# Performance work log

Hardware: AMD Instinct MI355X
Metric: run time of the kernel (lower is better)

The kernel has to match this reference:

```python
import jax, jax.numpy as jnp
import numpy as np

K = 16  # neighbors

def setup_inputs() -> dict:
    key = jax.random.key(0)
    k1, k2, k3 = jax.random.split(key, 3)
    B, C_in, C_out, N = 4, 64, 64, 8192
    x = jax.random.normal(k1, (B, C_in, N), dtype=jnp.float32)
    coords = jax.random.normal(k2, (B, 3, N), dtype=jnp.float32)
    W = jax.random.normal(k3, (C_out, C_in), dtype=jnp.float32) * 0.05
    return {"x": x, "coords": coords, "W": W}


def _knn_indices(coords, k):
    # coords: [B, 3, N]; squared pairwise distances d[b,i,j] = ||c_i - c_j||^2
    sq = jnp.sum(coords * coords, axis=1)                      # [B, N]
    inner = jnp.einsum('bdi,bdj->bij', coords, coords)         # [B, N, N]
    dist = sq[:, :, None] + sq[:, None, :] - 2.0 * inner       # [B, N, N]
    # k smallest distances -> top_k of negated distances
    _, idx = jax.lax.top_k(-dist, k)                           # [B, N, k]
    return idx


def _gather_neighbors(x, idx):
    # x: [B, C, N], idx: [B, N, k] -> [B, C, N, k]
    return jax.vmap(lambda xb, ib: xb[:, ib])(x, idx)


def reference(x, coords, W):
    idx = _knn_indices(coords, K)                              # [B, N, k]
    knn_x = _gather_neighbors(x, idx)                          # [B, C_in, N, k]
    # PointwiseConv2D (1x1 conv, no bias) == channel matmul
    mlp = jnp.einsum('oc,bcnk->bonk', W, knn_x)                # [B, C_out, N, k]
    y = jnp.max(mlp, axis=-1)                                  # [B, C_out, N]
    return (y, coords)
```

## Files before the change

kernel.cpp:

```cpp
#include <hip/hip_runtime.h>

#define BB 4
#define NN 8192
#define QB 32
#define NW 8
#define CAP 96
#define SLACK 6e-3f

typedef unsigned long long u64;
typedef unsigned int u32;
typedef _Float16 f16x8 __attribute__((ext_vector_type(8)));
typedef float f32x16 __attribute__((ext_vector_type(16)));

__device__ __forceinline__ u64 shfl_xor_u64(u64 v, int m) {
  u32 lo = (u32)v, hi = (u32)(v >> 32);
  lo = (u32)__shfl_xor((int)lo, m, 64);
  hi = (u32)__shfl_xor((int)hi, m, 64);
  return ((u64)hi << 32) | lo;
}
__device__ __forceinline__ u64 shfl_u64(u64 v, int src) {
  u32 lo = (u32)v, hi = (u32)(v >> 32);
  lo = (u32)__shfl((int)lo, src, 64);
  hi = (u32)__shfl((int)hi, src, 64);
  return ((u64)hi << 32) | lo;
}
__device__ __forceinline__ u64 min_u64(u64 a, u64 b) { return a < b ? a : b; }
__device__ __forceinline__ float rfl(float x) {
  return __int_as_float(__builtin_amdgcn_readfirstlane(__float_as_int(x)));
}

__device__ __forceinline__ u64 bitonic64(u64 v, int lane) {
#pragma unroll
  for (int k = 2; k <= 64; k <<= 1) {
#pragma unroll
    for (int jm = k >> 1; jm >= 1; jm >>= 1) {
      u64 o = shfl_xor_u64(v, jm);
      bool keepmin = ((lane & jm) == 0) == ((lane & k) == 0);
      u64 mn = min_u64(v, o);
      u64 mx = (v < o) ? o : v;
      v = keepmin ? mn : mx;
    }
  }
  return v;
}

__device__ __forceinline__ float dist_exact(float qx, float qy, float qz, float qw,
                                            float cx, float cy, float cz, float cw) {
#pragma clang fp contract(off)
  float inner = qx * cx;
  inner = inner + qy * cy;
  inner = inner + qz * cz;
  float tt = qw + cw;
  return __builtin_fmaf(-2.0f, inner, tt);
}

__global__ void fused_prep_zmat(const float* __restrict__ x, const float* __restrict__ W,
                                const float* __restrict__ coords,
                                float* __restrict__ z, float4* __restrict__ c4p,
                                _Float16* __restrict__ bfr,
                                float* __restrict__ ycoords) {
#pragma clang fp contract(off)
  __shared__ float Ws[64 * 65];
  __shared__ float xs[64 * 32];
  int t = threadIdx.x;
  if (blockIdx.x < 1024) {
    int blk = blockIdx.x;
    int b = blk >> 8;
    int j0 = (blk & 255) * 32;
    for (int r = t; r < 4096; r += 256) Ws[(r >> 6) * 65 + (r & 63)] = W[r];
    const float* xb = x + (size_t)b * 64 * NN;
    for (int r = 0; r < 8; ++r) {
      int idx = t + r * 256;
      int c = idx >> 5, j = idx & 31;
      xs[c * 32 + j] = xb[(size_t)c * NN + j0 + j];
    }
    __syncthreads();
    int o = t & 63, jb = (t >> 6) * 8;
    float acc[8];
#pragma unroll
    for (int m = 0; m < 8; ++m) acc[m] = 0.f;
    for (int c = 0; c < 64; ++c) {
      float w = Ws[o * 65 + c];
#pragma unroll
      for (int m = 0; m < 8; ++m) acc[m] = __builtin_fmaf(w, xs[c * 32 + jb + m], acc[m]);
    }
#pragma unroll
    for (int m = 0; m < 8; ++m)
      z[((size_t)b * NN + j0 + jb + m) * 64 + o] = acc[m];
  } else {
    int t2 = (blockIdx.x - 1024) * 256 + t;
    int b = t2 >> 13;
    int i = t2 & (NN - 1);
    const float* cb = coords + (size_t)b * 3 * NN;
    float cx = cb[i];
    float cy = cb[NN + i];
    float cz = cb[2 * NN + i];
    float sq = (cx * cx + cy * cy) + cz * cz;
    float4 v; v.x = -2.0f * cx; v.y = -2.0f * cy; v.z = -2.0f * cz; v.w = sq;
    c4p[t2] = v;

    _Float16 xh = (_Float16)v.x, yh = (_Float16)v.y, zh = (_Float16)v.z;
    _Float16 xl = (_Float16)(v.x - (float)xh);
    _Float16 yl = (_Float16)(v.y - (float)yh);
    _Float16 zl = (_Float16)(v.z - (float)zh);
    _Float16 sh = (_Float16)sq;
    _Float16 sl = (_Float16)(sq - (float)sh);
    f16x8 b0, b1;
    b0[0] = xh; b0[1] = xh; b0[2] = xl; b0[3] = yh;
    b0[4] = yh; b0[5] = yl; b0[6] = zh; b0[7] = zh;
    b1[0] = zl; b1[1] = sh; b1[2] = sl;
    b1[3] = (_Float16)0.f; b1[4] = (_Float16)0.f; b1[5] = (_Float16)0.f;
    b1[6] = (_Float16)0.f; b1[7] = (_Float16)0.f;
    f16x8* bp = (f16x8*)bfr;
    bp[(size_t)t2 * 2]     = b0;
    bp[(size_t)t2 * 2 + 1] = b1;

#pragma unroll
    for (int r = 0; r < 3; ++r)
      ycoords[r * (BB * NN) + t2] = coords[r * (BB * NN) + t2];
  }
}

__global__ void __launch_bounds__(512, 8) knn_gather(const float4* __restrict__ c4p,
                                                     const _Float16* __restrict__ bfr,
                                                     const float* __restrict__ z,
                                                     float* __restrict__ y) {
  __shared__ __align__(16) char pool[QB * 128 * 4];
  __shared__ float TfL[QB];
  __shared__ int scnt[QB];
  __shared__ int sidx[QB][16];
  __shared__ float ys[64][QB + 1];
  float (*wmin)[128] = (float(*)[128])pool;
  u32 (*survj)[CAP] = (u32(*)[CAP])pool;

  int t = threadIdx.x;
  int w = t >> 6, lane = t & 63;
  int lq = lane & 31, lg = lane >> 5;
  int lg4 = lg << 2;
  int qbase = blockIdx.x * QB;
  int b = qbase >> 13;
  int i0 = qbase & (NN - 1);
  const float4* cp = c4p + (size_t)b * NN;
  int wbase = w * (NN / NW);

  if (t < QB) scnt[t] = 0;

  float4 qv = cp[i0 + lq];
  float qx = -0.5f * qv.x, qy = -0.5f * qv.y, qz = -0.5f * qv.z;
  _Float16 xh = (_Float16)qx, yh = (_Float16)qy, zh = (_Float16)qz;
  _Float16 xl = (_Float16)(qx - (float)xh);
  _Float16 yl = (_Float16)(qy - (float)yh);
  _Float16 zl = (_Float16)(qz - (float)zh);
  f16x8 af;
  if (lg == 0) {
    af[0] = xh; af[1] = xl; af[2] = xh; af[3] = yh;
    af[4] = yl; af[5] = yh; af[6] = zh; af[7] = zl;
  } else {
    af[0] = zh; af[1] = (_Float16)1.0f; af[2] = (_Float16)1.0f;
    af[3] = (_Float16)0.f; af[4] = (_Float16)0.f; af[5] = (_Float16)0.f;
    af[6] = (_Float16)0.f; af[7] = (_Float16)0.f;
  }

  f32x16 zzz, mn;
#pragma unroll
  for (int r = 0; r < 16; ++r) { zzz[r] = 0.f; mn[r] = 3.402823466e+38f; }

  const f16x8* lp = (const f16x8*)bfr + (((size_t)b * NN + wbase + lq) * 2 + lg);

#pragma unroll 2
  for (int tt = 0; tt < 32; tt += 2) {
    f16x8 bc0 = lp[tt * 64];
    f16x8 bc1 = lp[(tt + 1) * 64];
    f32x16 d0 = __builtin_amdgcn_mfma_f32_32x32x16_f16(af, bc0, zzz, 0, 0, 0);
    f32x16 d1 = __builtin_amdgcn_mfma_f32_32x32x16_f16(af, bc1, zzz, 0, 0, 0);
#pragma unroll
    for (int r = 0; r < 16; ++r) mn[r] = fminf(fminf(mn[r], d0[r]), d1[r]);
  }

#pragma unroll
  for (int r = 0; r < 16; ++r) {
    float m2 = fminf(mn[r], __shfl_xor(mn[r], 16, 64));
    int q = (r & 3) + 8 * (r >> 2) + lg4;
    if (lq < 16) wmin[q][w * 16 + lq] = m2;
  }
  __syncthreads();

#pragma unroll 1
  for (int qi = 0; qi < QB / NW; ++qi) {
    int q = w * (QB / NW) + qi;
    float v = fminf(wmin[q][2 * lane], wmin[q][2 * lane + 1]);
#pragma unroll
    for (int k = 2; k <= 64; k <<= 1) {
#pragma unroll
      for (int jm = k >> 1; jm >= 1; jm >>= 1) {
        float o = __shfl_xor(v, jm, 64);
        bool keepmin = ((lane & jm) == 0) == ((lane & k) == 0);
        v = keepmin ? fminf(v, o) : fmaxf(v, o);
      }
    }
    if (lane == 15) TfL[q] = v + SLACK;
  }
  __syncthreads();

  f32x16 mc;
#pragma unroll
  for (int r = 0; r < 16; ++r) mc[r] = -TfL[(r & 3) + 8 * (r >> 2) + lg4];

#pragma unroll 2
  for (int tt = 0; tt < 32; ++tt) {
    f16x8 bc = lp[tt * 64];
    f32x16 d = __builtin_amdgcn_mfma_f32_32x32x16_f16(af, bc, mc, 0, 0, 0);
    int cand = wbase + tt * 32 + lq;
#pragma unroll
    for (int r = 0; r < 16; ++r) {
      if (d[r] <= 0.f) {
        int q = (r & 3) + 8 * (r >> 2) + lg4;
        int pos = atomicAdd(&scnt[q], 1);
        if (pos < CAP) survj[q][pos] = (u32)cand;
      }
    }
  }
  __syncthreads();

  const float* zb = z + (size_t)b * NN * 64;
#pragma unroll 1
  for (int qi = 0; qi < QB / NW; ++qi) {
    int q = w * (QB / NW) + qi;
    int n = scnt[q]; if (n > CAP) n = CAP;
    float4 qq = cp[i0 + q];
    float eqx = rfl(-0.5f * qq.x), eqy = rfl(-0.5f * qq.y);
    float eqz = rfl(-0.5f * qq.z), eqw = rfl(qq.w);
    u64 v = ~0ull;
    if (lane < n) {
      int c = (int)survj[q][lane];
      float4 cj = cp[c];
      float de = dist_exact(eqx, eqy, eqz, eqw,
                            -0.5f * cj.x, -0.5f * cj.y, -0.5f * cj.z, cj.w);
      u32 f = __float_as_uint(de);
      u32 m32 = f ^ ((u32)(((int)f) >> 31) | 0x80000000u);
      v = ((u64)m32 << 32) | (u32)c;
    }
    v = bitonic64(v, lane);
    if (n > 64) {
      u64 v2 = ~0ull;
      if (lane + 64 < n) {
        int c = (int)survj[q][lane + 64];
        float4 cj = cp[c];
        float de = dist_exact(eqx, eqy, eqz, eqw,
                              -0.5f * cj.x, -0.5f * cj.y, -0.5f * cj.z, cj.w);
        u32 f = __float_as_uint(de);
        u32 m32 = f ^ ((u32)(((int)f) >> 31) | 0x80000000u);
        v2 = ((u64)m32 << 32) | (u32)c;
      }
      v2 = bitonic64(v2, lane);
      u64 vm = (lane < 16) ? v : ((lane < 32) ? shfl_u64(v2, lane - 16) : ~0ull);
      v = bitonic64(vm, lane);
    }
    if (lane < 16) sidx[q][lane] = (int)(v & 0xFFFFFFFFull);
  }

#pragma unroll 1
  for (int qi = 0; qi < QB / NW; ++qi) {
    int q = w * (QB / NW) + qi;
    const int* id = sidx[q];
    float m = -3.402823466e+38f;
#pragma unroll
    for (int k = 0; k < 16; ++k)
      m = fmaxf(m, zb[(size_t)id[k] * 64 + lane]);
    ys[lane][q] = m;
  }
  __syncthreads();
  {
    int o = t >> 3;
    int ql0 = (t & 7) * 4;
    float4 vv;
    vv.x = ys[o][ql0]; vv.y = ys[o][ql0 + 1];
    vv.z = ys[o][ql0 + 2]; vv.w = ys[o][ql0 + 3];
    *(float4*)&y[((size_t)b * 64 + o) * NN + i0 + ql0] = vv;
  }
}

extern "C" void kernel_launch(void* const* d_in, const int* in_sizes, int n_in,
                              void* d_out, int out_size, void* d_ws, size_t ws_size,
                              hipStream_t stream) {
  const float* x      = (const float*)d_in[0];
  const float* coords = (const float*)d_in[1];
  const float* W      = (const float*)d_in[2];
  float* y = (float*)d_out;

  char* ws = (char*)d_ws;
  float4*   c4p = (float4*)ws;
  _Float16* bfr = (_Float16*)(ws + (512u << 10));
  float*    z   = (float*)(ws + (2u << 20));

  float* ycoords = y + (size_t)BB * 64 * NN;

  fused_prep_zmat<<<1024 + 128, 256, 0, stream>>>(x, W, coords, z, c4p, bfr, ycoords);
  knn_gather<<<BB * NN / QB, 512, 0, stream>>>(c4p, bfr, z, y);
}
```

Before: 137.7 us.

## Register-tile the z matmul and sample fewer candidates for the kNN threshold

The prep kernel's channel matmul moves to 64-point blocks with a 4x4 register tile per thread. It reads a transposed, padded W and x tiles from shared memory as float4 and writes z with float4 stores, which halves the prep grid. In the kNN kernel, the first pass that estimates each query's distance threshold now scans only half the candidate tiles, and the survivor-collection loop is unrolled further. The shuffle used when merging the two sorted survivor halves is now done by every lane instead of inside a divergent select. Sampling fewer candidates gives a looser threshold, so more points survive, which risks overflowing the fixed survivor capacity and costs extra exact-distance sorting work.

```diff
diff --git a/kernel.cpp b/kernel.cpp
--- a/kernel.cpp
+++ b/kernel.cpp
@@ -54,41 +54,59 @@
   return __builtin_fmaf(-2.0f, inner, tt);
 }
 
-__global__ void fused_prep_zmat(const float* __restrict__ x, const float* __restrict__ W,
-                                const float* __restrict__ coords,
-                                float* __restrict__ z, float4* __restrict__ c4p,
-                                _Float16* __restrict__ bfr,
-                                float* __restrict__ ycoords) {
+__global__ void __launch_bounds__(256, 4) fused_prep_zmat(
+    const float* __restrict__ x, const float* __restrict__ W,
+    const float* __restrict__ coords,
+    float* __restrict__ z, float4* __restrict__ c4p,
+    _Float16* __restrict__ bfr,
+    float* __restrict__ ycoords) {
 #pragma clang fp contract(off)
-  __shared__ float Ws[64 * 65];
-  __shared__ float xs[64 * 32];
+  __shared__ float Wst[64 * 68];
+  __shared__ float xs[64 * 64];
   int t = threadIdx.x;
-  if (blockIdx.x < 1024) {
+  if (blockIdx.x < 512) {
     int blk = blockIdx.x;
-    int b = blk >> 8;
-    int j0 = (blk & 255) * 32;
-    for (int r = t; r < 4096; r += 256) Ws[(r >> 6) * 65 + (r & 63)] = W[r];
+    int b = blk >> 7;
+    int j0 = (blk & 127) * 64;
+    for (int r = t; r < 4096; r += 256) Wst[(r & 63) * 68 + (r >> 6)] = W[r];
     const float* xb = x + (size_t)b * 64 * NN;
-    for (int r = 0; r < 8; ++r) {
+#pragma unroll
+    for (int r = 0; r < 16; ++r) {
       int idx = t + r * 256;
-      int c = idx >> 5, j = idx & 31;
-      xs[c * 32 + j] = xb[(size_t)c * NN + j0 + j];
+      int c = idx >> 6, j = idx & 63;
+      xs[c * 64 + j] = xb[(size_t)c * NN + j0 + j];
     }
     __syncthreads();
-    int o = t & 63, jb = (t >> 6) * 8;
-    float acc[8];
-#pragma unroll
-    for (int m = 0; m < 8; ++m) acc[m] = 0.f;
+    int o0 = (t & 15) * 4, jb = (t >> 4) * 4;
+    float4 a0 = {0.f, 0.f, 0.f, 0.f}, a1 = a0, a2 = a0, a3 = a0;
+#pragma unroll 4
     for (int c = 0; c < 64; ++c) {
-      float w = Ws[o * 65 + c];
-#pragma unroll
-      for (int m = 0; m < 8; ++m) acc[m] = __builtin_fmaf(w, xs[c * 32 + jb + m], acc[m]);
-    }
-#pragma unroll
-    for (int m = 0; m < 8; ++m)
-      z[((size_t)b * NN + j0 + jb + m) * 64 + o] = acc[m];
+      float4 w4 = *(const float4*)&Wst[c * 68 + o0];
+      float4 x4 = *(const float4*)&xs[c * 64 + jb];
+      a0.x = __builtin_fmaf(w4.x, x4.x, a0.x);
+      a0.y = __builtin_fmaf(w4.y, x4.x, a0.y);
+      a0.z = __builtin_fmaf(w4.z, x4.x, a0.z);
+      a0.w = __builtin_fmaf(w4.w, x4.x, a0.w);
+      a1.x = __builtin_fmaf(w4.x, x4.y, a1.x);
+      a1.y = __builtin_fmaf(w4.y, x4.y, a1.y);
+      a1.z = __builtin_fmaf(w4.z, x4.y, a1.z);
+      a1.w = __builtin_fmaf(w4.w, x4.y, a1.w);
+      a2.x = __builtin_fmaf(w4.x, x4.z, a2.x);
+      a2.y = __builtin_fmaf(w4.y, x4.z, a2.y);
+      a2.z = __builtin_fmaf(w4.z, x4.z, a2.z);
+      a2.w = __builtin_fmaf(w4.w, x4.z, a2.w);
+      a3.x = __builtin_fmaf(w4.x, x4.w, a3.x);
+      a3.y = __builtin_fmaf(w4.y, x4.w, a3.y);
+      a3.z = __builtin_fmaf(w4.z, x4.w, a3.z);
+      a3.w = __builtin_fmaf(w4.w, x4.w, a3.w);
+    }
+    size_t rbase = (size_t)b * NN + j0 + jb;
+    *(float4*)&z[(rbase + 0) * 64 + o0] = a0;
+    *(float4*)&z[(rbase + 1) * 64 + o0] = a1;
+    *(float4*)&z[(rbase + 2) * 64 + o0] = a2;
+    *(float4*)&z[(rbase + 3) * 64 + o0] = a3;
   } else {
-    int t2 = (blockIdx.x - 1024) * 256 + t;
+    int t2 = (blockIdx.x - 512) * 256 + t;
     int b = t2 >> 13;
     int i = t2 & (NN - 1);
     const float* cb = coords + (size_t)b * 3 * NN;
@@ -168,7 +186,7 @@
   const f16x8* lp = (const f16x8*)bfr + (((size_t)b * NN + wbase + lq) * 2 + lg);
 
 #pragma unroll 2
-  for (int tt = 0; tt < 32; tt += 2) {
+  for (int tt = 0; tt < 16; tt += 2) {
     f16x8 bc0 = lp[tt * 64];
     f16x8 bc1 = lp[(tt + 1) * 64];
     f32x16 d0 = __builtin_amdgcn_mfma_f32_32x32x16_f16(af, bc0, zzz, 0, 0, 0);
@@ -206,7 +224,7 @@
 #pragma unroll
   for (int r = 0; r < 16; ++r) mc[r] = -TfL[(r & 3) + 8 * (r >> 2) + lg4];
 
-#pragma unroll 2
+#pragma unroll 4
   for (int tt = 0; tt < 32; ++tt) {
     f16x8 bc = lp[tt * 64];
     f32x16 d = __builtin_amdgcn_mfma_f32_32x32x16_f16(af, bc, mc, 0, 0, 0);
@@ -253,7 +271,8 @@
         v2 = ((u64)m32 << 32) | (u32)c;
       }
       v2 = bitonic64(v2, lane);
-      u64 vm = (lane < 16) ? v : ((lane < 32) ? shfl_u64(v2, lane - 16) : ~0ull);
+      u64 s2 = shfl_u64(v2, (lane + 48) & 63);
+      u64 vm = (lane < 16) ? v : ((lane < 32) ? s2 : ~0ull);
       v = bitonic64(vm, lane);
     }
     if (lane < 16) sidx[q][lane] = (int)(v & 0xFFFFFFFFull);
@@ -295,6 +314,6 @@
 
   float* ycoords = y + (size_t)BB * 64 * NN;
 
-  fused_prep_zmat<<<1024 + 128, 256, 0, stream>>>(x, W, coords, z, c4p, bfr, ycoords);
+  fused_prep_zmat<<<512 + 128, 256, 0, stream>>>(x, W, coords, z, c4p, bfr, ycoords);
   knn_gather<<<BB * NN / QB, 512, 0, stream>>>(c4p, bfr, z, y);
 }
```

After: 136.9 us. About the same (-0.6%).
